# Kernel tuning notes

Measured on AMD Instinct MI355X. Metric: run time of the kernel, lower is better.

## Reference

```python
import jax, jax.numpy as jnp
import numpy as np

N = 50000      # nodes
E0 = 400000    # random edges (before self loops)
F_IN = 64      # in_channels == out_channels (required by the view in forward)
H = 2          # heads
C = 64         # per-head out_channels
B, T = 1, 8
NEG_SLOPE = 0.2


def setup_inputs() -> dict:
    key = jax.random.key(0)
    ks = jax.random.split(key, 7)
    self_loops = jnp.arange(N, dtype=jnp.int32)  # GATConv add_self_loops=True
    src = jnp.concatenate([jax.random.randint(ks[0], (E0,), 0, N, dtype=jnp.int32), self_loops])
    dst = jnp.concatenate([jax.random.randint(ks[1], (E0,), 0, N, dtype=jnp.int32), self_loops])
    h = jax.random.normal(ks[2], (B, N, T, F_IN), dtype=jnp.float32)
    glorot = float(np.sqrt(2.0 / (F_IN + H * C)))
    W = jax.random.normal(ks[3], (F_IN, H, C), dtype=jnp.float32) * glorot
    att_src = jax.random.normal(ks[4], (H, C), dtype=jnp.float32) * 0.1
    att_dst = jax.random.normal(ks[5], (H, C), dtype=jnp.float32) * 0.1
    bias = jax.random.normal(ks[6], (C,), dtype=jnp.float32) * 0.1
    return {"h": h, "src": src, "dst": dst, "W": W,
            "att_src": att_src, "att_dst": att_dst, "bias": bias}


def _gat_step(xt, src, dst, W, att_src, att_dst, bias, n_nodes):
    # xt: [N, F_in] node features for one timestep
    xl = jnp.einsum('nf,fhc->nhc', xt, W)               # [N, H, C]
    a_s = jnp.einsum('nhc,hc->nh', xl, att_src)          # source score per node
    a_d = jnp.einsum('nhc,hc->nh', xl, att_dst)          # dest score per node
    e = jax.nn.leaky_relu(a_s[src] + a_d[dst], NEG_SLOPE)  # [E, H]
    # segment softmax over incoming edges of each destination node
    emax = jax.ops.segment_max(e, dst, num_segments=n_nodes)
    ex = jnp.exp(e - emax[dst])
    denom = jax.ops.segment_sum(ex, dst, num_segments=n_nodes)
    alpha = ex / denom[dst]                              # [E, H]
    msg = alpha[:, :, None] * xl[src]                    # [E, H, C]
    out = jax.ops.segment_sum(msg, dst, num_segments=n_nodes)  # [N, H, C]
    out = out.mean(axis=1) + bias                        # concat=False: head mean
    return jax.nn.elu(out)


def reference(h, src, dst, W, att_src, att_dst, bias):
    Bn, Nn, Tn, Fin = h.shape
    # [B, N, T, F] -> [B*T, N, F] (matches h.transpose(1,2).view(-1, N, F))
    x = jnp.transpose(h, (0, 2, 1, 3)).reshape(Bn * Tn, Nn, Fin)

    def step(carry, xt):
        return carry, _gat_step(xt, src, dst, W, att_src, att_dst, bias, Nn)

    _, outs = jax.lax.scan(step, None, x)                # [B*T, N, C]
    out = outs.reshape(Bn, Tn, Nn, -1)
    return jnp.transpose(out, (0, 2, 1, 3))              # [B, N, T, C]
```

## Files before the change

kernel.cpp:

```cpp
#include <hip/hip_runtime.h>
#include <hip/hip_bf16.h>
#include <math.h>

#define T_STEPS 8
#define F_IN 64
#define HC 128
#define C_OUT 64
#define NEG_SLOPE 0.2f

typedef _Float16 half8 __attribute__((ext_vector_type(8)));
typedef _Float16 half2v __attribute__((ext_vector_type(2)));

static __device__ __forceinline__ float dot2(half2v a, half2v b, float c) {
    return __builtin_amdgcn_fdot2(a, b, c, false);
}

__global__ void k_zero_i32(int* p, int n) {
    int i = blockIdx.x * blockDim.x + threadIdx.x;
    if (i < n) p[i] = 0;
}

__global__ void k_count(const int* __restrict__ dst, int* __restrict__ cnt, int E) {
    int e = blockIdx.x * blockDim.x + threadIdx.x;
    if (e < E) atomicAdd(&cnt[dst[e]], 1);
}

__global__ void k_scan1(int* data, int* bsum, int n) {
    __shared__ int tmp[256];
    int tid = threadIdx.x;
    int i = blockIdx.x * 256 + tid;
    int v = (i < n) ? data[i] : 0;
    tmp[tid] = v; __syncthreads();
    for (int off = 1; off < 256; off <<= 1) {
        int x = (tid >= off) ? tmp[tid - off] : 0;
        __syncthreads();
        tmp[tid] += x;
        __syncthreads();
    }
    if (i < n) data[i] = tmp[tid] - v;
    if (tid == 255) bsum[blockIdx.x] = tmp[255];
}

__global__ void k_scan2(int* bsum, int nb) {
    __shared__ int tmp[256];
    int tid = threadIdx.x;
    int v = (tid < nb) ? bsum[tid] : 0;
    tmp[tid] = v; __syncthreads();
    for (int off = 1; off < 256; off <<= 1) {
        int x = (tid >= off) ? tmp[tid - off] : 0;
        __syncthreads();
        tmp[tid] += x;
        __syncthreads();
    }
    if (tid < nb) bsum[tid] = tmp[tid] - v;
}

__global__ void k_scan3(int* data, const int* __restrict__ bsum, int* cursor, int n, int total) {
    int i = blockIdx.x * 256 + threadIdx.x;
    if (i < n) {
        int v = data[i] + bsum[i >> 8];
        data[i] = v;
        cursor[i] = v;
    }
    if (i == 0) data[n] = total;
}

__global__ void k_fill(const int* __restrict__ src, const int* __restrict__ dst,
                       int* __restrict__ cursor, int* __restrict__ csr_src, int E) {
    int e = blockIdx.x * blockDim.x + threadIdx.x;
    if (e < E) {
        int d = dst[e];
        int pos = atomicAdd(&cursor[d], 1);
        csr_src[pos] = src[e];
    }
}

__global__ __launch_bounds__(256) void k_gemm(
    const float* __restrict__ h, const float* __restrict__ W,
    const float* __restrict__ att_src, const float* __restrict__ att_dst,
    _Float16* __restrict__ xlh, float* __restrict__ a_s, float* __restrict__ a_d,
    int N)
{
    __shared__ float sW[F_IN * HC];
    __shared__ float sX[F_IN * 64];
    __shared__ float sAS[HC], sAD[HC];

    int tid = threadIdx.x;
    int t = blockIdx.y;
    int node0 = blockIdx.x * 64;
    _Float16* xlt = xlh + (size_t)t * N * HC;
    float* ast = a_s + (size_t)t * N * 2;
    float* adt = a_d + (size_t)t * N * 2;

    for (int i = tid * 4; i < F_IN * HC; i += 1024)
        *(float4*)&sW[i] = *(const float4*)&W[i];
    if (tid < HC) { sAS[tid] = att_src[tid]; sAD[tid] = att_dst[tid]; }

    for (int u = tid; u < 64 * 16; u += 256) {
        int nl = u >> 4;
        int f4 = u & 15;
        int n = node0 + nl;
        float4 v = make_float4(0.f, 0.f, 0.f, 0.f);
        if (n < N) v = *(const float4*)&h[(n * T_STEPS + t) * F_IN + f4 * 4];
        sX[(f4 * 4 + 0) * 64 + nl] = v.x;
        sX[(f4 * 4 + 1) * 64 + nl] = v.y;
        sX[(f4 * 4 + 2) * 64 + nl] = v.z;
        sX[(f4 * 4 + 3) * 64 + nl] = v.w;
    }
    __syncthreads();

    int tx = tid & 31;
    int ty = tid >> 5;
    int lane = tid & 63;
    float acc[8][4];
    #pragma unroll
    for (int i = 0; i < 8; i++)
        #pragma unroll
        for (int j = 0; j < 4; j++) acc[i][j] = 0.f;

    #pragma unroll 4
    for (int f = 0; f < F_IN; f++) {
        float4 wv = *(float4*)&sW[f * HC + tx * 4];
        float4 xa = *(float4*)&sX[f * 64 + ty * 8];
        float4 xb = *(float4*)&sX[f * 64 + ty * 8 + 4];
        float xs[8] = {xa.x, xa.y, xa.z, xa.w, xb.x, xb.y, xb.z, xb.w};
        #pragma unroll
        for (int i = 0; i < 8; i++) {
            acc[i][0] += xs[i] * wv.x;
            acc[i][1] += xs[i] * wv.y;
            acc[i][2] += xs[i] * wv.z;
            acc[i][3] += xs[i] * wv.w;
        }
    }

    float4 vs = *(float4*)&sAS[tx * 4];
    float4 vd = *(float4*)&sAD[tx * 4];
    #pragma unroll
    for (int i = 0; i < 8; i++) {
        int n = node0 + ty * 8 + i;
        float p0 = __shfl(acc[i][0], (lane + 16) & 63);
        float p1 = __shfl(acc[i][1], (lane + 16) & 63);
        float p2 = __shfl(acc[i][2], (lane + 16) & 63);
        float p3 = __shfl(acc[i][3], (lane + 16) & 63);
        if (tx < 16 && n < N) {
            half8 v;
            v[0] = (_Float16)acc[i][0]; v[1] = (_Float16)p0;
            v[2] = (_Float16)acc[i][1]; v[3] = (_Float16)p1;
            v[4] = (_Float16)acc[i][2]; v[5] = (_Float16)p2;
            v[6] = (_Float16)acc[i][3]; v[7] = (_Float16)p3;
            *(half8*)&xlt[(size_t)n * HC + tx * 8] = v;
        }
        float ps = acc[i][0] * vs.x + acc[i][1] * vs.y + acc[i][2] * vs.z + acc[i][3] * vs.w;
        float pd = acc[i][0] * vd.x + acc[i][1] * vd.y + acc[i][2] * vd.z + acc[i][3] * vd.w;
        #pragma unroll
        for (int off = 8; off >= 1; off >>= 1) {
            ps += __shfl_down(ps, off, 16);
            pd += __shfl_down(pd, off, 16);
        }
        if ((tx & 15) == 0 && n < N) {
            int hh = tx >> 4;
            ast[(size_t)n * 2 + hh] = ps;
            adt[(size_t)n * 2 + hh] = pd;
        }
    }
}

__global__ __launch_bounds__(256) void k_edge(
    const int* __restrict__ csr_row, const int* __restrict__ csr_src,
    const float* __restrict__ a_s, const float* __restrict__ a_d,
    const _Float16* __restrict__ xlh, const float* __restrict__ bias,
    float* __restrict__ out, int N)
{
    __shared__ int2 edata[16][16];

    int tid  = threadIdx.x;
    int lane = tid & 63;
    int wid  = tid >> 6;
    int grp  = lane >> 4;
    int gl   = lane & 15;
    int t = blockIdx.y;
    const _Float16* xlt = xlh + (size_t)t * N * HC;
    const float* ast = a_s + (size_t)t * N * 2;
    const float* adt = a_d + (size_t)t * N * 2;

    int nodeBlock0 = blockIdx.x * 16;
    int node = nodeBlock0 + wid * 4 + grp;
    bool nvalid = node < N;

    int beg = 0, end = 0;
    if (nvalid) { beg = csr_row[node]; end = csr_row[node + 1]; }
    int deg = end - beg;

    float bs = bias[lane];

    if (__ballot(deg > 16) == 0ull) {
        float2 adv = make_float2(0.f, 0.f);
        if (nvalid) adv = *(const float2*)&adt[(size_t)node * 2];

        int e = beg + gl;
        bool ev = nvalid && (e < end);
        int s = ev ? csr_src[e] : 0;
        float e0 = -1e30f, e1 = -1e30f;
        if (ev) {
            float2 asv = *(const float2*)&ast[(size_t)s * 2];
            e0 = asv.x + adv.x;
            e1 = asv.y + adv.y;
            e0 = e0 > 0.f ? e0 : NEG_SLOPE * e0;
            e1 = e1 > 0.f ? e1 : NEG_SLOPE * e1;
        }
        float m0 = e0, m1 = e1;
        #pragma unroll
        for (int off = 8; off >= 1; off >>= 1) {
            m0 = fmaxf(m0, __shfl_xor(m0, off));
            m1 = fmaxf(m1, __shfl_xor(m1, off));
        }
        float x0 = ev ? __expf(e0 - m0) : 0.f;
        float x1 = ev ? __expf(e1 - m1) : 0.f;
        float d0 = x0, d1 = x1;
        #pragma unroll
        for (int off = 8; off >= 1; off >>= 1) {
            d0 += __shfl_xor(d0, off);
            d1 += __shfl_xor(d1, off);
        }
        float w0 = x0 * (0.5f / d0);
        float w1 = x1 * (0.5f / d1);

        union { uint u; _Float16 hh[2]; } cw;
        cw.hh[0] = ev ? (_Float16)w0 : (_Float16)0.f;
        cw.hh[1] = ev ? (_Float16)w1 : (_Float16)0.f;
        edata[wid * 4 + grp][gl] = make_int2(ev ? s : 0, (int)cw.u);

        #pragma unroll
        for (int k = 0; k < 4; k++) {
            int nk = nodeBlock0 + wid * 4 + k;
            if (nk >= N) continue;
            int dk = __shfl(deg, k * 16);
            int dkr = (dk + 3) & ~3;
            float a0 = 0.f, a1 = 0.f;
            const int2* row = edata[wid * 4 + k];
            for (int j = 0; j < dkr; j += 4) {
                int4 p = *(const int4*)&row[j];
                int4 q = *(const int4*)&row[j + 2];
                half2v v0 = *(const half2v*)&xlt[(size_t)p.x * HC + lane * 2];
                half2v v1 = *(const half2v*)&xlt[(size_t)p.z * HC + lane * 2];
                half2v v2 = *(const half2v*)&xlt[(size_t)q.x * HC + lane * 2];
                half2v v3 = *(const half2v*)&xlt[(size_t)q.z * HC + lane * 2];
                union { int i; half2v h; } c0, c1, c2, c3;
                c0.i = p.y; c1.i = p.w;
                c2.i = q.y; c3.i = q.w;
                a0 = dot2(v0, c0.h, a0);
                a1 = dot2(v1, c1.h, a1);
                a0 = dot2(v2, c2.h, a0);
                a1 = dot2(v3, c3.h, a1);
            }
            float acc = a0 + a1 + bs;
            float o = acc > 0.f ? acc : expm1f(acc);
            out[((size_t)nk * T_STEPS + t) * C_OUT + lane] = o;
        }
    } else {
        #pragma unroll
        for (int k = 0; k < 4; k++) {
            int nk = nodeBlock0 + wid * 4 + k;
            if (nk >= N) continue;
            int bk = __shfl(beg, k * 16);
            int ek = __shfl(end, k * 16);
            float2 adv = *(const float2*)&adt[(size_t)nk * 2];

            float m0 = -1e30f, m1 = -1e30f;
            for (int e = bk + lane; e < ek; e += 64) {
                int s = csr_src[e];
                float2 asv = *(const float2*)&ast[(size_t)s * 2];
                float e0 = asv.x + adv.x, e1 = asv.y + adv.y;
                e0 = e0 > 0.f ? e0 : NEG_SLOPE * e0;
                e1 = e1 > 0.f ? e1 : NEG_SLOPE * e1;
                m0 = fmaxf(m0, e0); m1 = fmaxf(m1, e1);
            }
            #pragma unroll
            for (int off = 32; off >= 1; off >>= 1) {
                m0 = fmaxf(m0, __shfl_xor(m0, off));
                m1 = fmaxf(m1, __shfl_xor(m1, off));
            }
            float d0 = 0.f, d1 = 0.f;
            for (int e = bk + lane; e < ek; e += 64) {
                int s = csr_src[e];
                float2 asv = *(const float2*)&ast[(size_t)s * 2];
                float e0 = asv.x + adv.x, e1 = asv.y + adv.y;
                e0 = e0 > 0.f ? e0 : NEG_SLOPE * e0;
                e1 = e1 > 0.f ? e1 : NEG_SLOPE * e1;
                d0 += __expf(e0 - m0); d1 += __expf(e1 - m1);
            }
            #pragma unroll
            for (int off = 32; off >= 1; off >>= 1) {
                d0 += __shfl_xor(d0, off);
                d1 += __shfl_xor(d1, off);
            }
            float r0 = 0.5f / d0, r1 = 0.5f / d1;

            float a0 = 0.f, a1 = 0.f;
            for (int base = bk; base < ek; base += 64) {
                int e = base + lane;
                int cnt = min(64, ek - base);
                int s = 0;
                union { uint u; _Float16 hh[2]; } cw;
                cw.u = 0u;
                if (e < ek) {
                    s = csr_src[e];
                    float2 asv = *(const float2*)&ast[(size_t)s * 2];
                    float e0 = asv.x + adv.x, e1 = asv.y + adv.y;
                    e0 = e0 > 0.f ? e0 : NEG_SLOPE * e0;
                    e1 = e1 > 0.f ? e1 : NEG_SLOPE * e1;
                    cw.hh[0] = (_Float16)(__expf(e0 - m0) * r0);
                    cw.hh[1] = (_Float16)(__expf(e1 - m1) * r1);
                }
                int wv = (int)cw.u;
                for (int j = 0; j < cnt; j++) {
                    int sj = __shfl(s, j);
                    int wj = __shfl(wv, j);
                    union { int i; half2v h; } c; c.i = wj;
                    half2v v = *(const half2v*)&xlt[(size_t)sj * HC + lane * 2];
                    a0 = dot2(v, c.h, a0);
                }
            }
            float acc = a0 + a1 + bs;
            float o = acc > 0.f ? acc : expm1f(acc);
            out[((size_t)nk * T_STEPS + t) * C_OUT + lane] = o;
        }
    }
}

extern "C" void kernel_launch(void* const* d_in, const int* in_sizes, int n_in,
                              void* d_out, int out_size, void* d_ws, size_t ws_size,
                              hipStream_t stream)
{
    const float* h       = (const float*)d_in[0];
    const int*   src     = (const int*)d_in[1];
    const int*   dst     = (const int*)d_in[2];
    const float* W       = (const float*)d_in[3];
    const float* att_src = (const float*)d_in[4];
    const float* att_dst = (const float*)d_in[5];
    const float* bias    = (const float*)d_in[6];
    float* out = (float*)d_out;

    int N = in_sizes[0] / (T_STEPS * F_IN);
    int E = in_sizes[1];

    char* wsb = (char*)d_ws;
    size_t off = 0;
    auto alloc = [&](size_t bytes) -> char* {
        off = (off + 255) & ~(size_t)255;
        char* p = wsb + off;
        off += bytes;
        return p;
    };

    int* csr_row = (int*)alloc((size_t)(N + 1) * sizeof(int));
    int* cursor  = (int*)alloc((size_t)N * sizeof(int));
    int* bsum    = (int*)alloc(1024 * sizeof(int));
    int* csr_src = (int*)alloc((size_t)E * sizeof(int));
    float* a_s   = (float*)alloc((size_t)T_STEPS * N * 2 * sizeof(float));
    float* a_d   = (float*)alloc((size_t)T_STEPS * N * 2 * sizeof(float));
    _Float16* xlh = (_Float16*)alloc((size_t)T_STEPS * N * HC * sizeof(_Float16));

    int nb = (N + 255) / 256;
    k_zero_i32<<<(N + 1 + 255) / 256, 256, 0, stream>>>(csr_row, N + 1);
    k_count<<<(E + 255) / 256, 256, 0, stream>>>(dst, csr_row, E);
    k_scan1<<<nb, 256, 0, stream>>>(csr_row, bsum, N);
    k_scan2<<<1, 256, 0, stream>>>(bsum, nb);
    k_scan3<<<nb, 256, 0, stream>>>(csr_row, bsum, cursor, N, E);
    k_fill<<<(E + 255) / 256, 256, 0, stream>>>(src, dst, cursor, csr_src, E);

    dim3 gg((N + 63) / 64, T_STEPS);
    k_gemm<<<gg, 256, 0, stream>>>(h, W, att_src, att_dst, xlh, a_s, a_d, N);
    dim3 ge((N + 15) / 16, T_STEPS);
    k_edge<<<ge, 256, 0, stream>>>(csr_row, csr_src, a_s, a_d, xlh, bias, out, N);
}
```

Baseline: 453.4 us.

## Rewrite projection GEMM with fp16 MFMA and fold attention vectors into weights

Replaces the scalar FP32 shared-memory GEMM in k_gemm with MFMA 16x16x32 fp16 instructions. Inputs and W are converted to fp16 and loaded straight into registers. A new tiny kernel precomputes W·att_src and W·att_dst so the attention scores come from one extra MFMA instead of a shuffle reduction. The output tile is staged through LDS in the interleaved head layout so stores to global memory are coalesced. The cost is lower precision for the inputs and the scores, plus one extra kernel launch.

```diff
diff --git a/kernel.cpp b/kernel.cpp
--- a/kernel.cpp
+++ b/kernel.cpp
@@ -10,6 +10,7 @@
 
 typedef _Float16 half8 __attribute__((ext_vector_type(8)));
 typedef _Float16 half2v __attribute__((ext_vector_type(2)));
+typedef float f32x4 __attribute__((ext_vector_type(4)));
 
 static __device__ __forceinline__ float dot2(half2v a, half2v b, float c) {
     return __builtin_amdgcn_fdot2(a, b, c, false);
@@ -75,93 +76,123 @@
     }
 }
 
+__global__ void k_wq(const float* __restrict__ W, const float* __restrict__ att_src,
+                     const float* __restrict__ att_dst, _Float16* __restrict__ WQt) {
+    int tid = threadIdx.x;
+    int q = tid & 3, f = tid >> 2;
+    const float* att = (q & 2) ? att_dst : att_src;
+    int hh = q & 1;
+    float s = 0.f;
+    #pragma unroll 8
+    for (int c = 0; c < 64; c++) s += W[f * HC + hh * 64 + c] * att[hh * 64 + c];
+    WQt[q * 64 + f] = (_Float16)s;
+}
+
 __global__ __launch_bounds__(256) void k_gemm(
     const float* __restrict__ h, const float* __restrict__ W,
-    const float* __restrict__ att_src, const float* __restrict__ att_dst,
+    const _Float16* __restrict__ WQt,
     _Float16* __restrict__ xlh, float* __restrict__ a_s, float* __restrict__ a_d,
     int N)
 {
-    __shared__ float sW[F_IN * HC];
-    __shared__ float sX[F_IN * 64];
-    __shared__ float sAS[HC], sAD[HC];
+    __shared__ _Float16 sOut[64 * HC];
 
     int tid = threadIdx.x;
     int t = blockIdx.y;
     int node0 = blockIdx.x * 64;
-    _Float16* xlt = xlh + (size_t)t * N * HC;
+    int w = tid >> 6;
+    int lane = tid & 63;
+    int cl = lane & 15;
+    int lg = lane >> 4;
+
+    half8 af[4][2];
+    #pragma unroll
+    for (int rt = 0; rt < 4; rt++) {
+        int n = node0 + rt * 16 + cl;
+        int nc = n < N ? n : N - 1;
+        const float* hp = h + ((size_t)nc * T_STEPS + t) * F_IN + lg * 8;
+        #pragma unroll
+        for (int ks = 0; ks < 2; ks++) {
+            f32x4 x0 = *(const f32x4*)(hp + ks * 32);
+            f32x4 x1 = *(const f32x4*)(hp + ks * 32 + 4);
+            half8 a;
+            a[0] = (_Float16)x0[0]; a[1] = (_Float16)x0[1];
+            a[2] = (_Float16)x0[2]; a[3] = (_Float16)x0[3];
+            a[4] = (_Float16)x1[0]; a[5] = (_Float16)x1[1];
+            a[6] = (_Float16)x1[2]; a[7] = (_Float16)x1[3];
+            af[rt][ks] = a;
+        }
+    }
+
+    half8 bf[2][2];
+    #pragma unroll
+    for (int ct = 0; ct < 2; ct++) {
+        int col = w * 32 + ct * 16 + cl;
+        #pragma unroll
+        for (int ks = 0; ks < 2; ks++) {
+            half8 b;
+            #pragma unroll
+            for (int j = 0; j < 8; j++)
+                b[j] = (_Float16)W[(size_t)(ks * 32 + lg * 8 + j) * HC + col];
+            bf[ct][ks] = b;
+        }
+    }
+
+    half8 bq[2];
+    #pragma unroll
+    for (int ks = 0; ks < 2; ks++) {
+        half8 b = {};
+        if (cl < 4) b = *(const half8*)&WQt[cl * 64 + lg * 8 + ks * 32];
+        bq[ks] = b;
+    }
+
+    f32x4 acc[4][2];
+    #pragma unroll
+    for (int rt = 0; rt < 4; rt++)
+        #pragma unroll
+        for (int ct = 0; ct < 2; ct++) {
+            f32x4 c = {0.f, 0.f, 0.f, 0.f};
+            c = __builtin_amdgcn_mfma_f32_16x16x32_f16(af[rt][0], bf[ct][0], c, 0, 0, 0);
+            c = __builtin_amdgcn_mfma_f32_16x16x32_f16(af[rt][1], bf[ct][1], c, 0, 0, 0);
+            acc[rt][ct] = c;
+        }
+
+    f32x4 sacc = {0.f, 0.f, 0.f, 0.f};
+    sacc = __builtin_amdgcn_mfma_f32_16x16x32_f16(af[w][0], bq[0], sacc, 0, 0, 0);
+    sacc = __builtin_amdgcn_mfma_f32_16x16x32_f16(af[w][1], bq[1], sacc, 0, 0, 0);
+
     float* ast = a_s + (size_t)t * N * 2;
     float* adt = a_d + (size_t)t * N * 2;
-
-    for (int i = tid * 4; i < F_IN * HC; i += 1024)
-        *(float4*)&sW[i] = *(const float4*)&W[i];
-    if (tid < HC) { sAS[tid] = att_src[tid]; sAD[tid] = att_dst[tid]; }
-
-    for (int u = tid; u < 64 * 16; u += 256) {
-        int nl = u >> 4;
-        int f4 = u & 15;
-        int n = node0 + nl;
-        float4 v = make_float4(0.f, 0.f, 0.f, 0.f);
-        if (n < N) v = *(const float4*)&h[(n * T_STEPS + t) * F_IN + f4 * 4];
-        sX[(f4 * 4 + 0) * 64 + nl] = v.x;
-        sX[(f4 * 4 + 1) * 64 + nl] = v.y;
-        sX[(f4 * 4 + 2) * 64 + nl] = v.z;
-        sX[(f4 * 4 + 3) * 64 + nl] = v.w;
-    }
+    if (cl < 4) {
+        float* basep = (cl & 2) ? adt : ast;
+        #pragma unroll
+        for (int reg = 0; reg < 4; reg++) {
+            int n = node0 + w * 16 + lg * 4 + reg;
+            if (n < N) basep[(size_t)n * 2 + (cl & 1)] = sacc[reg];
+        }
+    }
+
+    #pragma unroll
+    for (int rt = 0; rt < 4; rt++)
+        #pragma unroll
+        for (int ct = 0; ct < 2; ct++) {
+            int col = w * 32 + ct * 16 + cl;
+            int ei = (col & 63) * 2 + (col >> 6);
+            #pragma unroll
+            for (int reg = 0; reg < 4; reg++) {
+                int row = rt * 16 + lg * 4 + reg;
+                sOut[row * HC + ei] = (_Float16)acc[rt][ct][reg];
+            }
+        }
     __syncthreads();
 
-    int tx = tid & 31;
-    int ty = tid >> 5;
-    int lane = tid & 63;
-    float acc[8][4];
-    #pragma unroll
-    for (int i = 0; i < 8; i++)
-        #pragma unroll
-        for (int j = 0; j < 4; j++) acc[i][j] = 0.f;
-
-    #pragma unroll 4
-    for (int f = 0; f < F_IN; f++) {
-        float4 wv = *(float4*)&sW[f * HC + tx * 4];
-        float4 xa = *(float4*)&sX[f * 64 + ty * 8];
-        float4 xb = *(float4*)&sX[f * 64 + ty * 8 + 4];
-        float xs[8] = {xa.x, xa.y, xa.z, xa.w, xb.x, xb.y, xb.z, xb.w};
-        #pragma unroll
-        for (int i = 0; i < 8; i++) {
-            acc[i][0] += xs[i] * wv.x;
-            acc[i][1] += xs[i] * wv.y;
-            acc[i][2] += xs[i] * wv.z;
-            acc[i][3] += xs[i] * wv.w;
-        }
-    }
-
-    float4 vs = *(float4*)&sAS[tx * 4];
-    float4 vd = *(float4*)&sAD[tx * 4];
-    #pragma unroll
-    for (int i = 0; i < 8; i++) {
-        int n = node0 + ty * 8 + i;
-        float p0 = __shfl(acc[i][0], (lane + 16) & 63);
-        float p1 = __shfl(acc[i][1], (lane + 16) & 63);
-        float p2 = __shfl(acc[i][2], (lane + 16) & 63);
-        float p3 = __shfl(acc[i][3], (lane + 16) & 63);
-        if (tx < 16 && n < N) {
-            half8 v;
-            v[0] = (_Float16)acc[i][0]; v[1] = (_Float16)p0;
-            v[2] = (_Float16)acc[i][1]; v[3] = (_Float16)p1;
-            v[4] = (_Float16)acc[i][2]; v[5] = (_Float16)p2;
-            v[6] = (_Float16)acc[i][3]; v[7] = (_Float16)p3;
-            *(half8*)&xlt[(size_t)n * HC + tx * 8] = v;
-        }
-        float ps = acc[i][0] * vs.x + acc[i][1] * vs.y + acc[i][2] * vs.z + acc[i][3] * vs.w;
-        float pd = acc[i][0] * vd.x + acc[i][1] * vd.y + acc[i][2] * vd.z + acc[i][3] * vd.w;
-        #pragma unroll
-        for (int off = 8; off >= 1; off >>= 1) {
-            ps += __shfl_down(ps, off, 16);
-            pd += __shfl_down(pd, off, 16);
-        }
-        if ((tx & 15) == 0 && n < N) {
-            int hh = tx >> 4;
-            ast[(size_t)n * 2 + hh] = ps;
-            adt[(size_t)n * 2 + hh] = pd;
-        }
+    _Float16* xlt = xlh + (size_t)t * N * HC;
+    #pragma unroll
+    for (int it = 0; it < 4; it++) {
+        int idx = it * 256 + tid;
+        int row = idx >> 4;
+        int n = node0 + row;
+        if (n < N)
+            *(half8*)&xlt[(size_t)n * HC + (idx & 15) * 8] = *(half8*)&sOut[idx * 8];
     }
 }
 
@@ -359,6 +390,7 @@
     int* csr_src = (int*)alloc((size_t)E * sizeof(int));
     float* a_s   = (float*)alloc((size_t)T_STEPS * N * 2 * sizeof(float));
     float* a_d   = (float*)alloc((size_t)T_STEPS * N * 2 * sizeof(float));
+    _Float16* WQt = (_Float16*)alloc(4 * 64 * sizeof(_Float16));
     _Float16* xlh = (_Float16*)alloc((size_t)T_STEPS * N * HC * sizeof(_Float16));
 
     int nb = (N + 255) / 256;
@@ -369,8 +401,9 @@
     k_scan3<<<nb, 256, 0, stream>>>(csr_row, bsum, cursor, N, E);
     k_fill<<<(E + 255) / 256, 256, 0, stream>>>(src, dst, cursor, csr_src, E);
 
+    k_wq<<<1, 256, 0, stream>>>(W, att_src, att_dst, WQt);
     dim3 gg((N + 63) / 64, T_STEPS);
-    k_gemm<<<gg, 256, 0, stream>>>(h, W, att_src, att_dst, xlh, a_s, a_d, N);
+    k_gemm<<<gg, 256, 0, stream>>>(h, W, WQt, xlh, a_s, a_d, N);
     dim3 ge((N + 15) / 16, T_STEPS);
     k_edge<<<ge, 256, 0, stream>>>(csr_row, csr_src, a_s, a_d, xlh, bias, out, N);
 }
```

After: 488.8 us. 1.08x slower.
